# Performance work log

Measured on AMD Instinct MI355X. Metric: run time of the kernel, lower is better.

The kernel has to match this reference:

```python
import jax, jax.numpy as jnp
import numpy as np

N = 524288
MAXV = 8  # rect-rect intersection has at most 8 vertices
EPS = 1e-8


def setup_inputs() -> dict:
    key = jax.random.key(0)
    k1, k2, k3 = jax.random.split(key, 3)
    return {
        "box": jax.random.normal(k1, (N, 11), jnp.float32),
        "box_target": jax.random.normal(k2, (N, 11), jnp.float32),
        "weight": jax.random.uniform(k3, (N, 11), jnp.float32),
        "avg_factor": N // 2,
    }


def decode_box(box):
    # [x,y,z,logW,logL,logH,sin,cos,v...] -> [x,y,z,W,L,H,yaw,v...]
    yaw = jnp.arctan2(box[..., 6], box[..., 7])
    return jnp.concatenate(
        [box[..., :3], jnp.exp(box[..., 3:6]), yaw[..., None], box[..., 8:]], axis=-1)


def get_rect_vertices(bev):
    # bev: (5,) = [cx, cy, w, l, yaw] -> (4, 2) corners, CCW, rotated about center
    cx, cy, w, l, yaw = bev[0], bev[1], bev[2], bev[3], bev[4]
    dx, dy = w / 2, l / 2
    lx = jnp.stack([-dx, dx, dx, -dx])
    ly = jnp.stack([-dy, -dy, dy, dy])
    s, c = jnp.sin(yaw), jnp.cos(yaw)
    return jnp.stack([lx * c - ly * s + cx, lx * s + ly * c + cy], axis=-1)


def clip_halfplane(poly, count, a, b):
    # Sutherland-Hodgman clip of poly (MAXV,2) with `count` valid verts
    # against left side of directed edge a->b. Fixed-size buffer + mask.
    d = b - a  # (2,)
    idx = jnp.arange(MAXV)
    cnt = jnp.maximum(count, 1)
    prev = poly[(idx - 1) % cnt]
    cur = poly

    def is_left(p):
        return d[0] * (p[..., 1] - a[1]) - d[1] * (p[..., 0] - a[0]) >= 0

    cur_in, prev_in = is_left(cur), is_left(prev)
    num = (a[0] - prev[:, 0]) * d[1] - (a[1] - prev[:, 1]) * d[0]
    den = (cur[:, 0] - prev[:, 0]) * d[1] - (cur[:, 1] - prev[:, 1]) * d[0] + EPS
    ip = prev + (num / den)[:, None] * (cur - prev)  # edge/halfplane intersection
    valid = idx < count
    emit_ip = valid & (prev_in ^ cur_in)   # crossing edge -> emit intersection
    emit_cur = valid & cur_in              # inside vertex -> emit it
    # interleave per-input-edge outputs in original order (ip, then cur)
    pts = jnp.stack([ip, cur], axis=1).reshape(2 * MAXV, 2)
    emit = jnp.stack([emit_ip, emit_cur], axis=1).reshape(2 * MAXV)
    pos = jnp.where(emit, jnp.cumsum(emit) - 1, MAXV)  # compact valid pts to front
    out = jnp.zeros((MAXV, 2), poly.dtype).at[pos].set(
        jnp.where(emit[:, None], pts, 0.0), mode="drop")
    return out, jnp.minimum(emit.sum(), MAXV).astype(jnp.int32)


def poly_area(poly, count):
    # shoelace over the `count` valid vertices
    idx = jnp.arange(MAXV)
    nxt = poly[(idx + 1) % jnp.maximum(count, 1)]
    cross = jnp.where(idx < count, poly[:, 0] * nxt[:, 1] - poly[:, 1] * nxt[:, 0], 0.0)
    return jnp.abs(cross.sum() / 2.0)


def giou_one(bev1, bev2):
    v1 = get_rect_vertices(bev1)  # (4,2)
    v2 = get_rect_vertices(bev2)
    poly = jnp.zeros((MAXV, 2), bev1.dtype).at[:4].set(v1)
    count = jnp.int32(4)
    for i in range(4):  # clip subject rect by 4 half-planes of clip rect
        poly, count = clip_halfplane(poly, count, v2[i], v2[(i + 1) % 4])
        count = jnp.where(count < 3, 0, count)  # degenerate -> empty (original break)
    inter = poly_area(poly, count)
    area1 = bev1[2] * bev1[3]
    area2 = bev2[2] * bev2[3]
    union = area1 + area2 - inter
    allp = jnp.concatenate([v1, v2], axis=0)
    enclosing = (allp[:, 0].max() - allp[:, 0].min()) * (allp[:, 1].max() - allp[:, 1].min())
    iou = inter / (union + EPS)
    return iou - (enclosing - union) / (enclosing + EPS)


def _bev(dec):
    return jnp.stack([dec[:, 0], dec[:, 1], dec[:, 3], dec[:, 4], dec[:, 6]], axis=-1)


def reference(box, box_target, weight, avg_factor):
    af = max(float(avg_factor), 1.0)
    # L1 box loss (reg_weights are all 1.0 per init defaults)
    loss_box = (jnp.abs(box - box_target) * weight).sum() / af
    # rotated BEV GIoU loss
    bev_p = _bev(decode_box(box))
    bev_t = _bev(decode_box(box_target))
    giou = jax.vmap(giou_one)(bev_p, bev_t)
    loss_giou = (1.0 - giou).sum() / af
    return loss_box, loss_giou
```

## Files before the change

kernel.cpp:

```cpp
#include <hip/hip_runtime.h>

#define BLOCK 256
#define EPSF 1e-8f

typedef float f4u __attribute__((ext_vector_type(4), aligned(4)));

__device__ __forceinline__ void lb_clip(float px, float py, float dx, float dy,
                                        float hx, float hy,
                                        float& tmin, float& tmax) {
    float sdx = (fabsf(dx) > 1e-30f) ? dx : copysignf(1e-30f, dx);
    float sdy = (fabsf(dy) > 1e-30f) ? dy : copysignf(1e-30f, dy);
    float rdx = __frcp_rn(sdx);
    float rdy = __frcp_rn(sdy);
    float t1x = (-hx - px) * rdx, t2x = (hx - px) * rdx;
    float t1y = (-hy - py) * rdy, t2y = (hy - py) * rdy;
    tmin = fmaxf(fmaxf(fminf(t1x, t2x), fminf(t1y, t2y)), 0.f);
    tmax = fminf(fminf(fmaxf(t1x, t2x), fmaxf(t1y, t2y)), 1.f);
}

__global__ __launch_bounds__(BLOCK) void box_loss_main(
    const float* __restrict__ box, const float* __restrict__ tgt,
    const float* __restrict__ wgt, int n, float* __restrict__ partials)
{
    __shared__ float red[8];

    const int tid = threadIdx.x;
    const int i = blockIdx.x * BLOCK + tid;
    float sumL1 = 0.f, sumG = 0.f;

    if (i < n) {
        const float* bp = box + (size_t)i * 11;
        const float* tp = tgt + (size_t)i * 11;
        const float* wp = wgt + (size_t)i * 11;

        f4u b0 = *(const f4u*)(bp);
        f4u b1 = *(const f4u*)(bp + 4);
        f4u b2 = *(const f4u*)(bp + 7);
        f4u t0 = *(const f4u*)(tp);
        f4u t1 = *(const f4u*)(tp + 4);
        f4u t2 = *(const f4u*)(tp + 7);
        f4u w0 = *(const f4u*)(wp);
        f4u w1 = *(const f4u*)(wp + 4);
        f4u w2 = *(const f4u*)(wp + 7);

        float lb = 0.f;
        lb += fabsf(b0.x - t0.x) * w0.x;
        lb += fabsf(b0.y - t0.y) * w0.y;
        lb += fabsf(b0.z - t0.z) * w0.z;
        lb += fabsf(b0.w - t0.w) * w0.w;
        lb += fabsf(b1.x - t1.x) * w1.x;
        lb += fabsf(b1.y - t1.y) * w1.y;
        lb += fabsf(b1.z - t1.z) * w1.z;
        lb += fabsf(b1.w - t1.w) * w1.w;
        lb += fabsf(b2.y - t2.y) * w2.y;
        lb += fabsf(b2.z - t2.z) * w2.z;
        lb += fabsf(b2.w - t2.w) * w2.w;
        sumL1 = lb;

        float cx1 = b0.x, cy1 = b0.y, cx2 = t0.x, cy2 = t0.y;
        float w1v = __expf(b0.w), l1v = __expf(b1.x);
        float w2v = __expf(t0.w), l2v = __expf(t1.x);
        float r1 = rsqrtf(fmaxf(b1.z * b1.z + b1.w * b1.w, 1e-30f));
        float s1 = b1.z * r1, c1 = b1.w * r1;
        float r2 = rsqrtf(fmaxf(t1.z * t1.z + t1.w * t1.w, 1e-30f));
        float s2 = t1.z * r2, c2 = t1.w * r2;

        float hx1 = 0.5f * w1v, hy1 = 0.5f * l1v;
        float hx2 = 0.5f * w2v, hy2 = 0.5f * l2v;

        float e1x = fabsf(hx1 * c1) + fabsf(hy1 * s1);
        float e1y = fabsf(hx1 * s1) + fabsf(hy1 * c1);
        float e2x = fabsf(hx2 * c2) + fabsf(hy2 * s2);
        float e2y = fabsf(hx2 * s2) + fabsf(hy2 * c2);
        float enc = (fmaxf(cx1 + e1x, cx2 + e2x) - fminf(cx1 - e1x, cx2 - e2x))
                  * (fmaxf(cy1 + e1y, cy2 + e2y) - fminf(cy1 - e1y, cy2 - e2y));

        float dxw = cx1 - cx2, dyw = cy1 - cy2;
        float txl =  c2 * dxw + s2 * dyw;
        float tyl = -s2 * dxw + c2 * dyw;
        float cr_ = c1 * c2 + s1 * s2;
        float sr_ = s1 * c2 - c1 * s2;

        const float UX[4] = { -1.f, 1.f, 1.f, -1.f };
        const float UY[4] = { -1.f, -1.f, 1.f, 1.f };
        float qx[4], qy[4];
#pragma unroll
        for (int k = 0; k < 4; ++k) {
            float ux = UX[k] * hx1, uy = UY[k] * hy1;
            qx[k] = txl + ux * cr_ - uy * sr_;
            qy[k] = tyl + ux * sr_ + uy * cr_;
        }

        float inter2 = 0.f;
#pragma unroll
        for (int k = 0; k < 4; ++k) {
            int kn = (k + 1) & 3;
            float px = qx[k], py = qy[k];
            float dx = qx[kn] - px, dy = qy[kn] - py;
            float ta, tb;
            lb_clip(px, py, dx, dy, hx2, hy2, ta, tb);
            float ax = fmaf(ta, dx, px), ay = fmaf(ta, dy, py);
            float bx = fmaf(tb, dx, px), by = fmaf(tb, dy, py);
            float c = ax * by - ay * bx;
            inter2 += (tb > ta) ? c : 0.f;
        }
        {
            float Rx[4] = { -hx2, hx2, hx2, -hx2 };
            float Ry[4] = { -hy2, -hy2, hy2, hy2 };
            float ux[4], uy[4];
#pragma unroll
            for (int k = 0; k < 4; ++k) {
                float zx = Rx[k] - txl, zy = Ry[k] - tyl;
                ux[k] =  cr_ * zx + sr_ * zy;
                uy[k] = -sr_ * zx + cr_ * zy;
            }
#pragma unroll
            for (int k = 0; k < 4; ++k) {
                int kn = (k + 1) & 3;
                float du = ux[kn] - ux[k], dv = uy[kn] - uy[k];
                float ta, tb;
                lb_clip(ux[k], uy[k], du, dv, hx1, hy1, ta, tb);
                float dzx = Rx[kn] - Rx[k], dzy = Ry[kn] - Ry[k];
                float ax = fmaf(ta, dzx, Rx[k]), ay = fmaf(ta, dzy, Ry[k]);
                float bx = fmaf(tb, dzx, Rx[k]), by = fmaf(tb, dzy, Ry[k]);
                float c = ax * by - ay * bx;
                inter2 += (tb > ta) ? c : 0.f;
            }
        }
        float inter = 0.5f * fabsf(inter2);

        float areaU = w1v * l1v + w2v * l2v - inter;
        float iou = inter / (areaU + EPSF);
        float giou = iou - (enc - areaU) / (enc + EPSF);
        sumG = 1.f - giou;
    }

#pragma unroll
    for (int off = 32; off > 0; off >>= 1) {
        sumL1 += __shfl_down(sumL1, off);
        sumG  += __shfl_down(sumG, off);
    }
    const int wave = tid >> 6, lane = tid & 63;
    if (lane == 0) { red[wave] = sumL1; red[4 + wave] = sumG; }
    __syncthreads();
    if (tid == 0) {
        partials[2 * (size_t)blockIdx.x]     = red[0] + red[1] + red[2] + red[3];
        partials[2 * (size_t)blockIdx.x + 1] = red[4] + red[5] + red[6] + red[7];
    }
}

__global__ __launch_bounds__(256) void box_loss_final(
    const float* __restrict__ partials, int nblk,
    const int* __restrict__ avg_factor, float* __restrict__ out)
{
    __shared__ float red[8];
    float a = 0.f, g = 0.f;
    for (int i = threadIdx.x; i < nblk; i += 256) {
        a += partials[2 * (size_t)i];
        g += partials[2 * (size_t)i + 1];
    }
#pragma unroll
    for (int off = 32; off > 0; off >>= 1) {
        a += __shfl_down(a, off);
        g += __shfl_down(g, off);
    }
    const int wave = threadIdx.x >> 6, lane = threadIdx.x & 63;
    if (lane == 0) { red[wave] = a; red[4 + wave] = g; }
    __syncthreads();
    if (threadIdx.x == 0) {
        float af = (float)(*avg_factor);
        if (af < 1.f) af = 1.f;
        out[0] = (red[0] + red[1] + red[2] + red[3]) / af;
        out[1] = (red[4] + red[5] + red[6] + red[7]) / af;
    }
}

extern "C" void kernel_launch(void* const* d_in, const int* in_sizes, int n_in,
                              void* d_out, int out_size, void* d_ws, size_t ws_size,
                              hipStream_t stream) {
    const float* box = (const float*)d_in[0];
    const float* tgt = (const float*)d_in[1];
    const float* wgt = (const float*)d_in[2];
    const int*   af  = (const int*)d_in[3];
    float* out = (float*)d_out;
    float* partials = (float*)d_ws;

    int n = in_sizes[0] / 11;
    int nblk = (n + BLOCK - 1) / BLOCK;
    if (nblk < 1) nblk = 1;

    hipLaunchKernelGGL(box_loss_main, dim3(nblk), dim3(BLOCK), 0, stream,
                       box, tgt, wgt, n, partials);
    hipLaunchKernelGGL(box_loss_final, dim3(1), dim3(256), 0, stream,
                       partials, nblk, af, out);
}
```

Measured before the change: 22.08 us.

## Process four rows per thread with prefetch and simplify rectangle clipping algebra

Each thread now handles four rows strided by the grid size and loads the next row's data while computing the current one, so memory latency overlaps with math. The grid shrinks fourfold, which also shortens the final partials reduction. The edge clipping is rewritten to share reciprocals between opposite edges and to compute each edge's area contribution as clipped length times a cross product, cutting ALU work. The cost is higher register pressure from the prefetched rows and lower wave count, which could reduce occupancy.

```diff
diff --git a/kernel.cpp b/kernel.cpp
--- a/kernel.cpp
+++ b/kernel.cpp
@@ -1,138 +1,162 @@
 #include <hip/hip_runtime.h>
 
 #define BLOCK 256
+#define ITERS 4
 #define EPSF 1e-8f
 
 typedef float f4u __attribute__((ext_vector_type(4), aligned(4)));
 
-__device__ __forceinline__ void lb_clip(float px, float py, float dx, float dy,
-                                        float hx, float hy,
-                                        float& tmin, float& tmax) {
-    float sdx = (fabsf(dx) > 1e-30f) ? dx : copysignf(1e-30f, dx);
-    float sdy = (fabsf(dy) > 1e-30f) ? dy : copysignf(1e-30f, dy);
-    float rdx = __frcp_rn(sdx);
-    float rdy = __frcp_rn(sdy);
+struct Row9 { f4u b0, b1, b2, t0, t1, t2, w0, w1, w2; };
+
+__device__ __forceinline__ Row9 load_row(const float* __restrict__ box,
+                                         const float* __restrict__ tgt,
+                                         const float* __restrict__ wgt,
+                                         size_t r) {
+    Row9 R;
+    R.b0 = *(const f4u*)(box + r); R.b1 = *(const f4u*)(box + r + 4); R.b2 = *(const f4u*)(box + r + 7);
+    R.t0 = *(const f4u*)(tgt + r); R.t1 = *(const f4u*)(tgt + r + 4); R.t2 = *(const f4u*)(tgt + r + 7);
+    R.w0 = *(const f4u*)(wgt + r); R.w1 = *(const f4u*)(wgt + r + 4); R.w2 = *(const f4u*)(wgt + r + 7);
+    return R;
+}
+
+__device__ __forceinline__ float safe_rcp(float d) {
+    float sd = (fabsf(d) > 1e-30f) ? d : copysignf(1e-30f, d);
+    return __frcp_rn(sd);
+}
+
+__device__ __forceinline__ float clip_len(float px, float py,
+                                          float rdx, float rdy,
+                                          float hx, float hy) {
     float t1x = (-hx - px) * rdx, t2x = (hx - px) * rdx;
     float t1y = (-hy - py) * rdy, t2y = (hy - py) * rdy;
-    tmin = fmaxf(fmaxf(fminf(t1x, t2x), fminf(t1y, t2y)), 0.f);
-    tmax = fminf(fminf(fmaxf(t1x, t2x), fmaxf(t1y, t2y)), 1.f);
+    float tmin = fmaxf(fmaxf(fminf(t1x, t2x), fminf(t1y, t2y)), 0.f);
+    float tmax = fminf(fminf(fmaxf(t1x, t2x), fmaxf(t1y, t2y)), 1.f);
+    return fmaxf(tmax - tmin, 0.f);
+}
+
+__device__ __forceinline__ void box_compute(const Row9& R, float& l1out, float& gout)
+{
+    f4u b0 = R.b0, b1 = R.b1, b2 = R.b2;
+    f4u t0 = R.t0, t1 = R.t1, t2 = R.t2;
+    f4u w0 = R.w0, w1 = R.w1, w2 = R.w2;
+
+    float lb = 0.f;
+    lb += fabsf(b0.x - t0.x) * w0.x;
+    lb += fabsf(b0.y - t0.y) * w0.y;
+    lb += fabsf(b0.z - t0.z) * w0.z;
+    lb += fabsf(b0.w - t0.w) * w0.w;
+    lb += fabsf(b1.x - t1.x) * w1.x;
+    lb += fabsf(b1.y - t1.y) * w1.y;
+    lb += fabsf(b1.z - t1.z) * w1.z;
+    lb += fabsf(b1.w - t1.w) * w1.w;
+    lb += fabsf(b2.y - t2.y) * w2.y;
+    lb += fabsf(b2.z - t2.z) * w2.z;
+    lb += fabsf(b2.w - t2.w) * w2.w;
+    l1out = lb;
+
+    float cx1 = b0.x, cy1 = b0.y, cx2 = t0.x, cy2 = t0.y;
+    float w1v = __expf(b0.w), l1v = __expf(b1.x);
+    float w2v = __expf(t0.w), l2v = __expf(t1.x);
+    float r1 = rsqrtf(fmaxf(b1.z * b1.z + b1.w * b1.w, 1e-30f));
+    float s1 = b1.z * r1, c1 = b1.w * r1;
+    float r2 = rsqrtf(fmaxf(t1.z * t1.z + t1.w * t1.w, 1e-30f));
+    float s2 = t1.z * r2, c2 = t1.w * r2;
+
+    float hx1 = 0.5f * w1v, hy1 = 0.5f * l1v;
+    float hx2 = 0.5f * w2v, hy2 = 0.5f * l2v;
+
+    float e1x = fabsf(hx1 * c1) + fabsf(hy1 * s1);
+    float e1y = fabsf(hx1 * s1) + fabsf(hy1 * c1);
+    float e2x = fabsf(hx2 * c2) + fabsf(hy2 * s2);
+    float e2y = fabsf(hx2 * s2) + fabsf(hy2 * c2);
+    float enc = (fmaxf(cx1 + e1x, cx2 + e2x) - fminf(cx1 - e1x, cx2 - e2x))
+              * (fmaxf(cy1 + e1y, cy2 + e2y) - fminf(cy1 - e1y, cy2 - e2y));
+
+    float dxw = cx1 - cx2, dyw = cy1 - cy2;
+    float txl =  c2 * dxw + s2 * dyw;
+    float tyl = -s2 * dxw + c2 * dyw;
+    float cr_ = c1 * c2 + s1 * s2;
+    float sr_ = s1 * c2 - c1 * s2;
+
+    float ax_ = hx1 * cr_, ay_ = hx1 * sr_;
+    float bx_ = hy1 * sr_, by_ = hy1 * cr_;
+    float q0x = txl - ax_ + bx_, q0y = tyl - ay_ - by_;
+    float q1x = txl + ax_ + bx_, q1y = tyl + ay_ - by_;
+    float q2x = txl + ax_ - bx_, q2y = tyl + ay_ + by_;
+    float q3x = txl - ax_ - bx_, q3y = tyl - ay_ + by_;
+
+    float inter2 = 0.f;
+
+    {
+        float d01x = 2.f * ax_, d01y = 2.f * ay_;
+        float d12x = -2.f * bx_, d12y = 2.f * by_;
+        float r01x = safe_rcp(d01x), r01y = safe_rcp(d01y);
+        float r12x = safe_rcp(d12x), r12y = safe_rcp(d12y);
+
+        float L0 = clip_len(q0x, q0y,  r01x,  r01y, hx2, hy2);
+        inter2 += L0 * (q0x * d01y - q0y * d01x);
+        float L1 = clip_len(q1x, q1y,  r12x,  r12y, hx2, hy2);
+        inter2 += L1 * (q1x * d12y - q1y * d12x);
+        float L2 = clip_len(q2x, q2y, -r01x, -r01y, hx2, hy2);
+        inter2 += L2 * (q2y * d01x - q2x * d01y);
+        float L3 = clip_len(q3x, q3y, -r12x, -r12y, hx2, hy2);
+        inter2 += L3 * (q3y * d12x - q3x * d12y);
+    }
+
+    {
+        float zx = -hx2 - txl, zy = -hy2 - tyl;
+        float u0x =  cr_ * zx + sr_ * zy;
+        float u0y = -sr_ * zx + cr_ * zy;
+        float E0x =  2.f * hx2 * cr_, E0y = -2.f * hx2 * sr_;
+        float E1x =  2.f * hy2 * sr_, E1y =  2.f * hy2 * cr_;
+        float u1x = u0x + E0x, u1y = u0y + E0y;
+        float u2x = u1x + E1x, u2y = u1y + E1y;
+        float u3x = u0x + E1x, u3y = u0y + E1y;
+        float re0x = safe_rcp(E0x), re0y = safe_rcp(E0y);
+        float re1x = safe_rcp(E1x), re1y = safe_rcp(E1y);
+
+        float tsum = 0.f;
+        tsum += clip_len(u0x, u0y,  re0x,  re0y, hx1, hy1);
+        tsum += clip_len(u1x, u1y,  re1x,  re1y, hx1, hy1);
+        tsum += clip_len(u2x, u2y, -re0x, -re0y, hx1, hy1);
+        tsum += clip_len(u3x, u3y, -re1x, -re1y, hx1, hy1);
+        inter2 += 2.f * hx2 * hy2 * tsum;
+    }
+
+    float inter = 0.5f * fabsf(inter2);
+    float areaU = w1v * l1v + w2v * l2v - inter;
+    float iou = inter / (areaU + EPSF);
+    float giou = iou - (enc - areaU) / (enc + EPSF);
+    gout = 1.f - giou;
 }
 
 __global__ __launch_bounds__(BLOCK) void box_loss_main(
     const float* __restrict__ box, const float* __restrict__ tgt,
-    const float* __restrict__ wgt, int n, float* __restrict__ partials)
+    const float* __restrict__ wgt, int n, int T, float* __restrict__ partials)
 {
     __shared__ float red[8];
 
     const int tid = threadIdx.x;
-    const int i = blockIdx.x * BLOCK + tid;
+    int i = blockIdx.x * BLOCK + tid;
     float sumL1 = 0.f, sumG = 0.f;
 
-    if (i < n) {
-        const float* bp = box + (size_t)i * 11;
-        const float* tp = tgt + (size_t)i * 11;
-        const float* wp = wgt + (size_t)i * 11;
-
-        f4u b0 = *(const f4u*)(bp);
-        f4u b1 = *(const f4u*)(bp + 4);
-        f4u b2 = *(const f4u*)(bp + 7);
-        f4u t0 = *(const f4u*)(tp);
-        f4u t1 = *(const f4u*)(tp + 4);
-        f4u t2 = *(const f4u*)(tp + 7);
-        f4u w0 = *(const f4u*)(wp);
-        f4u w1 = *(const f4u*)(wp + 4);
-        f4u w2 = *(const f4u*)(wp + 7);
-
-        float lb = 0.f;
-        lb += fabsf(b0.x - t0.x) * w0.x;
-        lb += fabsf(b0.y - t0.y) * w0.y;
-        lb += fabsf(b0.z - t0.z) * w0.z;
-        lb += fabsf(b0.w - t0.w) * w0.w;
-        lb += fabsf(b1.x - t1.x) * w1.x;
-        lb += fabsf(b1.y - t1.y) * w1.y;
-        lb += fabsf(b1.z - t1.z) * w1.z;
-        lb += fabsf(b1.w - t1.w) * w1.w;
-        lb += fabsf(b2.y - t2.y) * w2.y;
-        lb += fabsf(b2.z - t2.z) * w2.z;
-        lb += fabsf(b2.w - t2.w) * w2.w;
-        sumL1 = lb;
-
-        float cx1 = b0.x, cy1 = b0.y, cx2 = t0.x, cy2 = t0.y;
-        float w1v = __expf(b0.w), l1v = __expf(b1.x);
-        float w2v = __expf(t0.w), l2v = __expf(t1.x);
-        float r1 = rsqrtf(fmaxf(b1.z * b1.z + b1.w * b1.w, 1e-30f));
-        float s1 = b1.z * r1, c1 = b1.w * r1;
-        float r2 = rsqrtf(fmaxf(t1.z * t1.z + t1.w * t1.w, 1e-30f));
-        float s2 = t1.z * r2, c2 = t1.w * r2;
-
-        float hx1 = 0.5f * w1v, hy1 = 0.5f * l1v;
-        float hx2 = 0.5f * w2v, hy2 = 0.5f * l2v;
-
-        float e1x = fabsf(hx1 * c1) + fabsf(hy1 * s1);
-        float e1y = fabsf(hx1 * s1) + fabsf(hy1 * c1);
-        float e2x = fabsf(hx2 * c2) + fabsf(hy2 * s2);
-        float e2y = fabsf(hx2 * s2) + fabsf(hy2 * c2);
-        float enc = (fmaxf(cx1 + e1x, cx2 + e2x) - fminf(cx1 - e1x, cx2 - e2x))
-                  * (fmaxf(cy1 + e1y, cy2 + e2y) - fminf(cy1 - e1y, cy2 - e2y));
-
-        float dxw = cx1 - cx2, dyw = cy1 - cy2;
-        float txl =  c2 * dxw + s2 * dyw;
-        float tyl = -s2 * dxw + c2 * dyw;
-        float cr_ = c1 * c2 + s1 * s2;
-        float sr_ = s1 * c2 - c1 * s2;
-
-        const float UX[4] = { -1.f, 1.f, 1.f, -1.f };
-        const float UY[4] = { -1.f, -1.f, 1.f, 1.f };
-        float qx[4], qy[4];
+    bool v = i < n;
+    Row9 cur = load_row(box, tgt, wgt, (size_t)(v ? i : 0) * 11);
+
 #pragma unroll
-        for (int k = 0; k < 4; ++k) {
-            float ux = UX[k] * hx1, uy = UY[k] * hy1;
-            qx[k] = txl + ux * cr_ - uy * sr_;
-            qy[k] = tyl + ux * sr_ + uy * cr_;
+    for (int k = 0; k < ITERS; ++k) {
+        int inext = i + T;
+        bool vnext = false;
+        Row9 nxt;
+        if (k + 1 < ITERS) {
+            vnext = inext < n;
+            nxt = load_row(box, tgt, wgt, (size_t)(vnext ? inext : 0) * 11);
         }
-
-        float inter2 = 0.f;
-#pragma unroll
-        for (int k = 0; k < 4; ++k) {
-            int kn = (k + 1) & 3;
-            float px = qx[k], py = qy[k];
-            float dx = qx[kn] - px, dy = qy[kn] - py;
-            float ta, tb;
-            lb_clip(px, py, dx, dy, hx2, hy2, ta, tb);
-            float ax = fmaf(ta, dx, px), ay = fmaf(ta, dy, py);
-            float bx = fmaf(tb, dx, px), by = fmaf(tb, dy, py);
-            float c = ax * by - ay * bx;
-            inter2 += (tb > ta) ? c : 0.f;
-        }
-        {
-            float Rx[4] = { -hx2, hx2, hx2, -hx2 };
-            float Ry[4] = { -hy2, -hy2, hy2, hy2 };
-            float ux[4], uy[4];
-#pragma unroll
-            for (int k = 0; k < 4; ++k) {
-                float zx = Rx[k] - txl, zy = Ry[k] - tyl;
-                ux[k] =  cr_ * zx + sr_ * zy;
-                uy[k] = -sr_ * zx + cr_ * zy;
-            }
-#pragma unroll
-            for (int k = 0; k < 4; ++k) {
-                int kn = (k + 1) & 3;
-                float du = ux[kn] - ux[k], dv = uy[kn] - uy[k];
-                float ta, tb;
-                lb_clip(ux[k], uy[k], du, dv, hx1, hy1, ta, tb);
-                float dzx = Rx[kn] - Rx[k], dzy = Ry[kn] - Ry[k];
-                float ax = fmaf(ta, dzx, Rx[k]), ay = fmaf(ta, dzy, Ry[k]);
-                float bx = fmaf(tb, dzx, Rx[k]), by = fmaf(tb, dzy, Ry[k]);
-                float c = ax * by - ay * bx;
-                inter2 += (tb > ta) ? c : 0.f;
-            }
-        }
-        float inter = 0.5f * fabsf(inter2);
-
-        float areaU = w1v * l1v + w2v * l2v - inter;
-        float iou = inter / (areaU + EPSF);
-        float giou = iou - (enc - areaU) / (enc + EPSF);
-        sumG = 1.f - giou;
+        float l1, g;
+        box_compute(cur, l1, g);
+        sumL1 += v ? l1 : 0.f;
+        sumG  += v ? g  : 0.f;
+        if (k + 1 < ITERS) { cur = nxt; v = vnext; i = inext; }
     }
 
 #pragma unroll
@@ -186,11 +210,12 @@
     float* partials = (float*)d_ws;
 
     int n = in_sizes[0] / 11;
-    int nblk = (n + BLOCK - 1) / BLOCK;
+    int nblk = (n + BLOCK * ITERS - 1) / (BLOCK * ITERS);
     if (nblk < 1) nblk = 1;
+    int T = nblk * BLOCK;
 
     hipLaunchKernelGGL(box_loss_main, dim3(nblk), dim3(BLOCK), 0, stream,
-                       box, tgt, wgt, n, partials);
+                       box, tgt, wgt, n, T, partials);
     hipLaunchKernelGGL(box_loss_final, dim3(1), dim3(256), 0, stream,
                        partials, nblk, af, out);
 }
```

Result: faster. 19.63 us (-11.1%).
